# Optimization experiments

Hardware: AMD Instinct MI355X
Metric: run time of the kernel (lower is better)

The kernel has to match this reference:

```python
import jax, jax.numpy as jnp
import numpy as np

EMBED_DIM = 1024
NUM_HEADS = 16
HEAD_DIM = EMBED_DIM // NUM_HEADS


def setup_inputs() -> dict:
    key = jax.random.key(0)
    ks = jax.random.split(key, 6)
    B, S = 2, 2048
    x = jax.random.normal(ks[0], (B, S, EMBED_DIM), dtype=jnp.float32)
    # causal boolean mask, broadcast to (B, H, S, S)
    causal = jnp.tril(jnp.ones((S, S), dtype=bool))
    mask = jnp.broadcast_to(causal, (B, NUM_HEADS, S, S))
    s_in = 1.0 / np.sqrt(EMBED_DIM)
    qkv_w = jax.random.normal(ks[1], (3 * EMBED_DIM, EMBED_DIM), dtype=jnp.float32) * s_in
    qkv_b = jax.random.normal(ks[2], (3 * EMBED_DIM,), dtype=jnp.float32) * 0.01
    proj_w = jax.random.normal(ks[3], (EMBED_DIM, EMBED_DIM), dtype=jnp.float32) * s_in
    proj_b = jax.random.normal(ks[4], (EMBED_DIM,), dtype=jnp.float32) * 0.01
    return {"x": x, "mask": mask, "qkv_w": qkv_w, "qkv_b": qkv_b,
            "proj_w": proj_w, "proj_b": proj_b}


def reference(x, mask, qkv_w, qkv_b, proj_w, proj_b):
    B, S, E = x.shape
    H, D = NUM_HEADS, HEAD_DIM
    qkv = x @ qkv_w.T + qkv_b                     # (B, S, 3E)
    q, k, v = jnp.split(qkv, 3, axis=-1)
    # (B, H, S, D)
    q = q.reshape(B, S, H, D).transpose(0, 2, 1, 3)
    k = k.reshape(B, S, H, D).transpose(0, 2, 1, 3)
    v = v.reshape(B, S, H, D).transpose(0, 2, 1, 3)
    scale = D ** (-0.5)
    attn = jnp.einsum('bhqd,bhkd->bhqk', q, k) * scale
    attn = jnp.where(mask, attn, jnp.float32(-10000.0))
    attn = attn - jnp.max(attn, axis=-1, keepdims=True)
    attn = jax.nn.softmax(attn, axis=-1)
    attn = jnp.where(mask, attn, jnp.float32(0.0))
    # dropout is identity in eval mode
    out = jnp.einsum('bhqk,bhkd->bhqd', attn, v)
    out = out.transpose(0, 2, 1, 3).reshape(B, S, E)
    return out @ proj_w.T + proj_b
```

## Files before the change

### kernel.cpp

```cpp
#include <hip/hip_runtime.h>
#include <hip/hip_bf16.h>

#define BATCH 2
#define SEQ 2048
#define EMBED 1024
#define NHEADS 16
#define HDIM 64

typedef __hip_bfloat16 bf16;
typedef __attribute__((ext_vector_type(8))) short bf16x8;
typedef __attribute__((ext_vector_type(4))) short bf16x4;
typedef __attribute__((ext_vector_type(4))) float f32x4;

typedef const __attribute__((address_space(1))) void* gaddr_t;
typedef __attribute__((address_space(3))) void* laddr_t;

__device__ __forceinline__ bf16x8 lds_frag8(const bf16* p) {
    const bf16x4 a = *(const bf16x4*)p;
    const bf16x4 b = *(const bf16x4*)(p + 4);
    return __builtin_shufflevector(a, b, 0, 1, 2, 3, 4, 5, 6, 7);
}

__global__ __launch_bounds__(256)
void f2b_all(const float* __restrict__ s0, bf16* __restrict__ d0, int n0,
             const float* __restrict__ s1, bf16* __restrict__ d1, int n1,
             const float* __restrict__ s2, bf16* __restrict__ d2, int n2)
{
    int i = blockIdx.x * 256 + threadIdx.x;
    const float* s; bf16* d;
    if (i < n0)                { s = s0; d = d0; }
    else if ((i -= n0) < n1)   { s = s1; d = d1; }
    else if ((i -= n1) < n2)   { s = s2; d = d2; }
    else return;
    const float4 v = ((const float4*)s)[i];
    union { ushort4 u4; bf16 h[4]; } o;
    o.h[0] = __float2bfloat16(v.x);
    o.h[1] = __float2bfloat16(v.y);
    o.h[2] = __float2bfloat16(v.z);
    o.h[3] = __float2bfloat16(v.w);
    ((ushort4*)d)[i] = o.u4;
}

template<int MODE>
__global__ __launch_bounds__(256)
void gemm_bt(const bf16* __restrict__ A, const bf16* __restrict__ B,
             const float* __restrict__ bias, void* __restrict__ Cv,
             int M, int N, int K)
{
    __shared__ __align__(16) bf16 lA[128 * 32];
    __shared__ __align__(16) bf16 lB[128 * 32];
    const int tid  = threadIdx.x;
    const int bn   = blockIdx.x, bm = blockIdx.y;
    const int wave = tid >> 6, lane = tid & 63;
    const int wm   = (wave >> 1) << 6, wn = (wave & 1) << 6;
    const int quad = lane >> 4, l16 = lane & 15;

    f32x4 acc[4][4] = {};

    for (int kt = 0; kt < K; kt += 32) {
        __syncthreads();
        #pragma unroll
        for (int i = 0; i < 2; ++i) {
            const int c = tid + (i << 8);
            const int r = c >> 2, kc = (c & 3) << 3;
            const bf16* gA = A + (long)(bm * 128 + r) * K + (kt + kc);
            const bf16* gB = B + (long)(bn * 128 + r) * K + (kt + kc);
            __builtin_amdgcn_global_load_lds((gaddr_t)gA, (laddr_t)&lA[c << 3], 16, 0, 0);
            __builtin_amdgcn_global_load_lds((gaddr_t)gB, (laddr_t)&lB[c << 3], 16, 0, 0);
        }
        __syncthreads();

        bf16x8 af[4], bfr[4];
        #pragma unroll
        for (int t = 0; t < 4; ++t) {
            af[t]  = *(const bf16x8*)&lA[(wm + t * 16 + l16) * 32 + quad * 8];
            bfr[t] = *(const bf16x8*)&lB[(wn + t * 16 + l16) * 32 + quad * 8];
        }
        #pragma unroll
        for (int tm = 0; tm < 4; ++tm)
            #pragma unroll
            for (int tn = 0; tn < 4; ++tn)
                acc[tm][tn] = __builtin_amdgcn_mfma_f32_16x16x32_bf16(
                    af[tm], bfr[tn], acc[tm][tn], 0, 0, 0);
    }

    #pragma unroll
    for (int tm = 0; tm < 4; ++tm) {
        #pragma unroll
        for (int tn = 0; tn < 4; ++tn) {
            const int gn = bn * 128 + wn + tn * 16 + l16;
            const float bv = bias[gn];
            if (MODE == 0) {
                #pragma unroll
                for (int r = 0; r < 4; ++r) {
                    const int gm = bm * 128 + wm + tm * 16 + quad * 4 + r;
                    ((float*)Cv)[(long)gm * N + gn] = acc[tm][tn][r] + bv;
                }
            } else {
                const int part = gn >> 10, h = (gn >> 6) & (NHEADS - 1), d = gn & (HDIM - 1);
                const int gm0 = bm * 128 + wm + tm * 16 + quad * 4;
                const int b = gm0 >> 11, s0 = gm0 & (SEQ - 1);
                if (part == 2) {
                    union { ushort4 u4; bf16 hv[4]; } o;
                    #pragma unroll
                    for (int r = 0; r < 4; ++r) o.hv[r] = __float2bfloat16(acc[tm][tn][r] + bv);
                    const long off = ((((long)2 * BATCH + b) * NHEADS + h) * HDIM + d) * SEQ + s0;
                    *(ushort4*)((bf16*)Cv + off) = o.u4;
                } else {
                    #pragma unroll
                    for (int r = 0; r < 4; ++r) {
                        const long off = ((((long)part * BATCH + b) * NHEADS + h) * SEQ + (s0 + r)) * HDIM + d;
                        ((bf16*)Cv)[off] = __float2bfloat16(acc[tm][tn][r] + bv);
                    }
                }
            }
        }
    }
}

__global__ __launch_bounds__(256)
void attn_nf(const bf16* __restrict__ Q, const bf16* __restrict__ K,
             const bf16* __restrict__ Vt, float* __restrict__ Op,
             float* __restrict__ lp)
{
    __shared__ __align__(16) bf16 pS[4 * 32 * 68];

    const int tid  = threadIdx.x;
    const int wave = tid >> 6, lane = tid & 63;
    const int quad = lane >> 4, l15 = lane & 15;
    const int bh   = blockIdx.x;
    const int half = blockIdx.y >> 4;
    const int qidx = blockIdx.y & 15;
    const int qg   = (15 - qidx) * 4 + wave;
    const int qw0  = qg * 32;

    const bf16* Qb  = Q  + (long)bh * SEQ * HDIM;
    const bf16* Kb  = K  + (long)bh * SEQ * HDIM;
    const bf16* Vtb = Vt + (long)bh * HDIM * SEQ;
    bf16* pW = pS + wave * 32 * 68;

    bf16x8 qf[2][2];
    #pragma unroll
    for (int mt = 0; mt < 2; ++mt)
        #pragma unroll
        for (int c = 0; c < 2; ++c) {
            union { int4 i; bf16x8 v; } u;
            u.i = *(const int4*)(Qb + (long)(qw0 + mt * 16 + l15) * HDIM + c * 32 + quad * 8);
            qf[mt][c] = u.v;
        }

    f32x4 acc[2][4] = {};
    float lsum[8] = {};

    const int nkt = (qw0 >> 6) + 1;
    const float sc = 0.125f * 1.44269504088896340736f;

    for (int t = half; t < nkt; t += 2) {
        const int kb = t * 64;

        f32x4 s[2][4] = {};
        #pragma unroll
        for (int c = 0; c < 2; ++c) {
            #pragma unroll
            for (int nt = 0; nt < 4; ++nt) {
                union { int4 i; bf16x8 v; } u;
                u.i = *(const int4*)(Kb + (long)(kb + nt * 16 + l15) * HDIM + c * 32 + quad * 8);
                #pragma unroll
                for (int mt = 0; mt < 2; ++mt)
                    s[mt][nt] = __builtin_amdgcn_mfma_f32_16x16x32_bf16(
                        qf[mt][c], u.v, s[mt][nt], 0, 0, 0);
            }
        }

        #pragma unroll
        for (int mt = 0; mt < 2; ++mt)
            #pragma unroll
            for (int nt = 0; nt < 4; ++nt)
                #pragma unroll
                for (int r = 0; r < 4; ++r) {
                    const int rl = mt * 16 + quad * 4 + r;
                    const int cl = nt * 16 + l15;
                    const float p = ((kb + cl) <= (qw0 + rl))
                        ? __builtin_amdgcn_exp2f(s[mt][nt][r] * sc) : 0.f;
                    lsum[mt * 4 + r] += p;
                    pW[rl * 68 + cl] = __float2bfloat16(p);
                }

        #pragma unroll
        for (int c = 0; c < 2; ++c) {
            bf16x8 pf[2];
            #pragma unroll
            for (int mt = 0; mt < 2; ++mt)
                pf[mt] = lds_frag8(&pW[(mt * 16 + l15) * 68 + c * 32 + quad * 8]);
            #pragma unroll
            for (int nt = 0; nt < 4; ++nt) {
                union { int4 i; bf16x8 v; } u;
                u.i = *(const int4*)(Vtb + (long)(nt * 16 + l15) * SEQ + kb + c * 32 + quad * 8);
                #pragma unroll
                for (int mt = 0; mt < 2; ++mt)
                    acc[mt][nt] = __builtin_amdgcn_mfma_f32_16x16x32_bf16(
                        pf[mt], u.v, acc[mt][nt], 0, 0, 0);
            }
        }
    }

    #pragma unroll
    for (int i = 0; i < 8; ++i)
        #pragma unroll
        for (int m = 1; m < 16; m <<= 1) lsum[i] += __shfl_xor(lsum[i], m, 64);

    const long halfO = (long)BATCH * NHEADS * SEQ * HDIM;
    float* Oh = Op + half * halfO + ((long)bh * SEQ) * HDIM;
    float* lh = lp + half * (BATCH * NHEADS * SEQ) + bh * SEQ;
    #pragma unroll
    for (int mt = 0; mt < 2; ++mt)
        #pragma unroll
        for (int r = 0; r < 4; ++r) {
            const int rl = mt * 16 + quad * 4 + r;
            float* orow = Oh + (long)(qw0 + rl) * HDIM;
            #pragma unroll
            for (int nt = 0; nt < 4; ++nt)
                orow[nt * 16 + l15] = acc[mt][nt][r];
            if (l15 == 0) lh[qw0 + rl] = lsum[mt * 4 + r];
        }
}

__global__ __launch_bounds__(256)
void attn_combine(const float* __restrict__ Op, const float* __restrict__ lp,
                  bf16* __restrict__ att)
{
    const int i = blockIdx.x * 256 + threadIdx.x;
    const int d4 = i & 15, q = (i >> 4) & (SEQ - 1), bh = i >> 15;
    const long halfO = (long)BATCH * NHEADS * SEQ * HDIM;
    const long rowo  = ((long)bh * SEQ + q) * HDIM;
    const float4 a = ((const float4*)(Op + rowo))[d4];
    const float4 b = ((const float4*)(Op + halfO + rowo))[d4];
    const int li = bh * SEQ + q;
    const float inv = 1.f / (lp[li] + lp[BATCH * NHEADS * SEQ + li]);
    const int bb = bh >> 4, h = bh & 15;
    union { ushort4 u4; bf16 hv[4]; } o;
    o.hv[0] = __float2bfloat16((a.x + b.x) * inv);
    o.hv[1] = __float2bfloat16((a.y + b.y) * inv);
    o.hv[2] = __float2bfloat16((a.z + b.z) * inv);
    o.hv[3] = __float2bfloat16((a.w + b.w) * inv);
    *(ushort4*)(att + ((long)bb * SEQ + q) * EMBED + h * HDIM + d4 * 4) = o.u4;
}

extern "C" void kernel_launch(void* const* d_in, const int* in_sizes, int n_in,
                              void* d_out, int out_size, void* d_ws, size_t ws_size,
                              hipStream_t stream)
{
    const float* x      = (const float*)d_in[0];
    const float* qkv_w  = (const float*)d_in[2];
    const float* qkv_b  = (const float*)d_in[3];
    const float* proj_w = (const float*)d_in[4];
    const float* proj_b = (const float*)d_in[5];
    float* out = (float*)d_out;

    const long nX  = (long)BATCH * SEQ * EMBED;
    const long nQW = 3L * EMBED * EMBED;
    const long nPW = (long)EMBED * EMBED;
    const long per = (long)BATCH * NHEADS * SEQ * HDIM;

    bf16* xw  = (bf16*)d_ws;
    bf16* qwm = xw + nX;
    bf16* pwm = qwm + nQW;
    bf16* qw  = pwm + nPW;
    bf16* kw  = qw + per;
    bf16* vw  = kw + per;
    bf16* att = vw + per;
    float* Op = (float*)(att + per);
    float* lp = Op + 2 * per;

    const int n0 = (int)(nX / 4), n1 = (int)(nQW / 4), n2 = (int)(nPW / 4);
    f2b_all<<<(n0 + n1 + n2 + 255) / 256, 256, 0, stream>>>(
        x, xw, n0, qkv_w, qwm, n1, proj_w, pwm, n2);

    gemm_bt<1><<<dim3(3 * EMBED / 128, BATCH * SEQ / 128), 256, 0, stream>>>(
        xw, qwm, qkv_b, qw, BATCH * SEQ, 3 * EMBED, EMBED);

    attn_nf<<<dim3(BATCH * NHEADS, 32), 256, 0, stream>>>(qw, kw, vw, Op, lp);
    attn_combine<<<(int)(per / 4 / 256), 256, 0, stream>>>(Op, lp, att);

    gemm_bt<0><<<dim3(EMBED / 128, BATCH * SEQ / 128), 256, 0, stream>>>(
        att, pwm, proj_b, out, BATCH * SEQ, EMBED, EMBED);
}
```

Baseline: 724.5 us.

## Split attention key range three ways and interleave score/softmax per key subtile

Raises the key-dimension split of the no-max attention kernel from 2 to 3 partial outputs, launches 48 y-blocks per head, and makes the combine kernel sum three partials. The score computation is restructured to compute and exponentiate one 16-column subtile at a time, and launch bounds request 6 blocks per CU. The goal is more parallel blocks, better load balance across the causal triangle, and lower register pressure for higher occupancy. The cost is extra fp32 partial-output traffic and a heavier combine pass.

Measured after the change: 918.5 us. +26.8%, slower.

```diff
diff --git a/kernel.cpp b/kernel.cpp
--- a/kernel.cpp
+++ b/kernel.cpp
@@ -6,6 +6,7 @@
 #define EMBED 1024
 #define NHEADS 16
 #define HDIM 64
+#define NSPLIT 3
 
 typedef __hip_bfloat16 bf16;
 typedef __attribute__((ext_vector_type(8))) short bf16x8;
@@ -118,7 +119,7 @@
     }
 }
 
-__global__ __launch_bounds__(256)
+__global__ __launch_bounds__(256, 6)
 void attn_nf(const bf16* __restrict__ Q, const bf16* __restrict__ K,
              const bf16* __restrict__ Vt, float* __restrict__ Op,
              float* __restrict__ lp)
@@ -155,36 +156,33 @@
     const int nkt = (qw0 >> 6) + 1;
     const float sc = 0.125f * 1.44269504088896340736f;
 
-    for (int t = half; t < nkt; t += 2) {
+    for (int t = half; t < nkt; t += NSPLIT) {
         const int kb = t * 64;
 
-        f32x4 s[2][4] = {};
-        #pragma unroll
-        for (int c = 0; c < 2; ++c) {
-            #pragma unroll
-            for (int nt = 0; nt < 4; ++nt) {
+        #pragma unroll
+        for (int nt = 0; nt < 4; ++nt) {
+            f32x4 s2[2] = {};
+            #pragma unroll
+            for (int c = 0; c < 2; ++c) {
                 union { int4 i; bf16x8 v; } u;
                 u.i = *(const int4*)(Kb + (long)(kb + nt * 16 + l15) * HDIM + c * 32 + quad * 8);
                 #pragma unroll
                 for (int mt = 0; mt < 2; ++mt)
-                    s[mt][nt] = __builtin_amdgcn_mfma_f32_16x16x32_bf16(
-                        qf[mt][c], u.v, s[mt][nt], 0, 0, 0);
+                    s2[mt] = __builtin_amdgcn_mfma_f32_16x16x32_bf16(
+                        qf[mt][c], u.v, s2[mt], 0, 0, 0);
             }
-        }
-
-        #pragma unroll
-        for (int mt = 0; mt < 2; ++mt)
-            #pragma unroll
-            for (int nt = 0; nt < 4; ++nt)
+            #pragma unroll
+            for (int mt = 0; mt < 2; ++mt)
                 #pragma unroll
                 for (int r = 0; r < 4; ++r) {
                     const int rl = mt * 16 + quad * 4 + r;
                     const int cl = nt * 16 + l15;
                     const float p = ((kb + cl) <= (qw0 + rl))
-                        ? __builtin_amdgcn_exp2f(s[mt][nt][r] * sc) : 0.f;
+                        ? __builtin_amdgcn_exp2f(s2[mt][r] * sc) : 0.f;
                     lsum[mt * 4 + r] += p;
                     pW[rl * 68 + cl] = __float2bfloat16(p);
                 }
+        }
 
         #pragma unroll
         for (int c = 0; c < 2; ++c) {
@@ -233,17 +231,23 @@
     const int d4 = i & 15, q = (i >> 4) & (SEQ - 1), bh = i >> 15;
     const long halfO = (long)BATCH * NHEADS * SEQ * HDIM;
     const long rowo  = ((long)bh * SEQ + q) * HDIM;
-    const float4 a = ((const float4*)(Op + rowo))[d4];
-    const float4 b = ((const float4*)(Op + halfO + rowo))[d4];
     const int li = bh * SEQ + q;
-    const float inv = 1.f / (lp[li] + lp[BATCH * NHEADS * SEQ + li]);
-    const int bb = bh >> 4, h = bh & 15;
+    float4 a = ((const float4*)(Op + rowo))[d4];
+    float l = lp[li];
+    #pragma unroll
+    for (int h = 1; h < NSPLIT; ++h) {
+        const float4 b = ((const float4*)(Op + h * halfO + rowo))[d4];
+        a.x += b.x; a.y += b.y; a.z += b.z; a.w += b.w;
+        l += lp[h * (BATCH * NHEADS * SEQ) + li];
+    }
+    const float inv = 1.f / l;
+    const int bb = bh >> 4, hh = bh & 15;
     union { ushort4 u4; bf16 hv[4]; } o;
-    o.hv[0] = __float2bfloat16((a.x + b.x) * inv);
-    o.hv[1] = __float2bfloat16((a.y + b.y) * inv);
-    o.hv[2] = __float2bfloat16((a.z + b.z) * inv);
-    o.hv[3] = __float2bfloat16((a.w + b.w) * inv);
-    *(ushort4*)(att + ((long)bb * SEQ + q) * EMBED + h * HDIM + d4 * 4) = o.u4;
+    o.hv[0] = __float2bfloat16(a.x * inv);
+    o.hv[1] = __float2bfloat16(a.y * inv);
+    o.hv[2] = __float2bfloat16(a.z * inv);
+    o.hv[3] = __float2bfloat16(a.w * inv);
+    *(ushort4*)(att + ((long)bb * SEQ + q) * EMBED + hh * HDIM + d4 * 4) = o.u4;
 }
 
 extern "C" void kernel_launch(void* const* d_in, const int* in_sizes, int n_in,
@@ -270,7 +274,7 @@
     bf16* vw  = kw + per;
     bf16* att = vw + per;
     float* Op = (float*)(att + per);
-    float* lp = Op + 2 * per;
+    float* lp = Op + NSPLIT * per;
 
     const int n0 = (int)(nX / 4), n1 = (int)(nQW / 4), n2 = (int)(nPW / 4);
     f2b_all<<<(n0 + n1 + n2 + 255) / 256, 256, 0, stream>>>(
@@ -279,7 +283,7 @@
     gemm_bt<1><<<dim3(3 * EMBED / 128, BATCH * SEQ / 128), 256, 0, stream>>>(
         xw, qwm, qkv_b, qw, BATCH * SEQ, 3 * EMBED, EMBED);
 
-    attn_nf<<<dim3(BATCH * NHEADS, 32), 256, 0, stream>>>(qw, kw, vw, Op, lp);
+    attn_nf<<<dim3(BATCH * NHEADS, 16 * NSPLIT), 256, 0, stream>>>(qw, kw, vw, Op, lp);
     attn_combine<<<(int)(per / 4 / 256), 256, 0, stream>>>(Op, lp, att);
 
     gemm_bt<0><<<dim3(EMBED / 128, BATCH * SEQ / 128), 256, 0, stream>>>(
```
